# Kernel optimization log

Hardware: AMD Instinct MI355X
Metric: run time of the kernel (lower is better)

## Reference

```python
import jax, jax.numpy as jnp
import numpy as np

B, S, H, E = 4, 4096, 4096, 64
TOP_K = 2


def setup_inputs() -> dict:
    key = jax.random.key(0)
    k1, k2 = jax.random.split(key)
    x = jax.random.normal(k1, (B, S, H), dtype=jnp.float32)
    # nn.Linear weight: [num_experts, hidden_size]
    gate_w = jax.random.normal(k2, (E, H), dtype=jnp.float32) * (1.0 / np.sqrt(H))
    return {"x": x, "gate_w": gate_w}


def reference(x, gate_w):
    # gate linear: [B,S,H] @ [H,E] -> [B,S,E]
    router_logits = jnp.einsum("bsh,eh->bse", x, gate_w)
    router_weights = jax.nn.softmax(router_logits, axis=-1)
    topk_weights, topk_indices = jax.lax.top_k(router_weights, TOP_K)  # [B,S,2]
    topk_weights = topk_weights / jnp.sum(topk_weights, axis=-1, keepdims=True)
    return topk_weights, topk_indices
```

## Files before the change

### kernel.cpp

```cpp
#include <hip/hip_runtime.h>
#include <math.h>


constexpr int Hdim = 4096;
constexpr int Edim = 64;
constexpr int BM   = 64;
constexpr int BK   = 64;
constexpr int LSTR = 66;
constexpr int PSTR = 68;
constexpr int NKT  = Hdim / BK;
constexpr int NTOK = 16384;

__global__ __launch_bounds__(256)
void router_kernel(const float* __restrict__ x,
                   const float* __restrict__ gw,
                   float* __restrict__ out)
{
    __shared__ float lx[2 * BM * LSTR];
    __shared__ float lw[2 * Edim * LSTR];

    const int tid = threadIdx.x;
    const int t0  = blockIdx.x * BM;

    const int srow = tid >> 4;
    const int scol = (tid & 15) << 2;

    const int wave = tid >> 6, lane = tid & 63;
    const int tg = ((wave >> 1) << 3) + (lane >> 3);
    const int eg = ((wave & 1) << 3) + (lane & 7);

    float acc[4][4];
    #pragma unroll
    for (int i = 0; i < 4; ++i)
        #pragma unroll
        for (int j = 0; j < 4; ++j) acc[i][j] = 0.f;

    const float* xg = x + (size_t)t0 * Hdim;

    float4 rx[4], rw[4];
    #pragma unroll
    for (int m = 0; m < 4; ++m) {
        const int r = m * 16 + srow;
        rx[m] = *(const float4*)(xg + (size_t)r * Hdim + scol);
        rw[m] = *(const float4*)(gw + (size_t)r * Hdim + scol);
    }
    #pragma unroll
    for (int m = 0; m < 4; ++m) {
        const int r = m * 16 + srow;
        float2* px = (float2*)&lx[r * LSTR + scol];
        px[0] = make_float2(rx[m].x, rx[m].y);
        px[1] = make_float2(rx[m].z, rx[m].w);
        float2* pw = (float2*)&lw[r * LSTR + scol];
        pw[0] = make_float2(rw[m].x, rw[m].y);
        pw[1] = make_float2(rw[m].z, rw[m].w);
    }
    __syncthreads();

    for (int kt = 0; kt < NKT; ++kt) {
        const int cur = (kt & 1) ? BM * LSTR : 0;
        const int nxt = (kt & 1) ? 0 : BM * LSTR;
        const int knext = (kt + 1 < NKT) ? (kt + 1) * BK : 0;

        #pragma unroll
        for (int m = 0; m < 4; ++m) {
            const int r = m * 16 + srow;
            rx[m] = *(const float4*)(xg + (size_t)r * Hdim + knext + scol);
            rw[m] = *(const float4*)(gw + (size_t)r * Hdim + knext + scol);
        }

        const float* __restrict__ bx = &lx[cur];
        const float* __restrict__ bw = &lw[cur];
        #pragma unroll 8
        for (int k = 0; k < BK; k += 2) {
            float2 xa[4], wb[4];
            #pragma unroll
            for (int i = 0; i < 4; ++i)
                xa[i] = *(const float2*)&bx[(4 * tg + i) * LSTR + k];
            #pragma unroll
            for (int j = 0; j < 4; ++j)
                wb[j] = *(const float2*)&bw[(4 * eg + j) * LSTR + k];
            #pragma unroll
            for (int i = 0; i < 4; ++i)
                #pragma unroll
                for (int j = 0; j < 4; ++j)
                    acc[i][j] = fmaf(xa[i].y, wb[j].y,
                                 fmaf(xa[i].x, wb[j].x, acc[i][j]));
        }

        #pragma unroll
        for (int m = 0; m < 4; ++m) {
            const int r = m * 16 + srow;
            float2* px = (float2*)&lx[nxt + r * LSTR + scol];
            px[0] = make_float2(rx[m].x, rx[m].y);
            px[1] = make_float2(rx[m].z, rx[m].w);
            float2* pw = (float2*)&lw[nxt + r * LSTR + scol];
            pw[0] = make_float2(rw[m].x, rw[m].y);
            pw[1] = make_float2(rw[m].z, rw[m].w);
        }
        __syncthreads();
    }

    float* lg = lx;
    #pragma unroll
    for (int i = 0; i < 4; ++i) {
        float4 v = make_float4(acc[i][0], acc[i][1], acc[i][2], acc[i][3]);
        *(float4*)&lg[(4 * tg + i) * PSTR + 4 * eg] = v;
    }
    __syncthreads();

    if (tid < BM) {
        const float* row = &lg[tid * PSTR];
        float m1 = -INFINITY, m2 = -INFINITY;
        int i1 = 0, i2 = 0;
        for (int e = 0; e < Edim; ++e) {
            float v = row[e];
            if (v > m1) { m2 = m1; i2 = i1; m1 = v; i1 = e; }
            else if (v > m2) { m2 = v; i2 = e; }
        }
        const float r   = expf(m2 - m1);
        const float inv = 1.f / (1.f + r);
        const int t = t0 + tid;
        float* ow = out + 2 * (size_t)t;
        ow[0] = inv;
        ow[1] = r * inv;
        float* oi = out + 2 * (size_t)NTOK + 2 * (size_t)t;
        oi[0] = (float)i1;
        oi[1] = (float)i2;
    }
}

extern "C" void kernel_launch(void* const* d_in, const int* in_sizes, int n_in,
                              void* d_out, int out_size, void* d_ws, size_t ws_size,
                              hipStream_t stream) {
    const float* x  = (const float*)d_in[0];
    const float* gw = (const float*)d_in[1];
    float* out = (float*)d_out;
    dim3 grid(NTOK / BM), block(256);
    hipLaunchKernelGGL(router_kernel, grid, block, 0, stream, x, gw, out);
}
```

Measured before the change: 460.1 us.

## Compute router GEMM with split-fp16 MFMA instead of scalar FP32 FMAs

Replaces the scalar FP32 FMA inner loop with 16x16x32 fp16 MFMA instructions. Each FP32 input is split into a high fp16 part and a scaled low fp16 residual, and four MFMA products per tile are recombined so the result stays close to FP32 accuracy. Shared memory is reorganised into XOR-swizzled fp16 tiles to avoid bank conflicts. This trades extra conversion ALU work and four times the MFMA count for much higher matrix throughput, but it risks precision differences that could flip top-k ties.

```diff
diff --git a/kernel.cpp b/kernel.cpp
--- a/kernel.cpp
+++ b/kernel.cpp
@@ -1,115 +1,169 @@
 #include <hip/hip_runtime.h>
 #include <math.h>
 
+
+typedef _Float16 half8 __attribute__((ext_vector_type(8)));
+typedef float floatx4 __attribute__((ext_vector_type(4)));
 
 constexpr int Hdim = 4096;
 constexpr int Edim = 64;
 constexpr int BM   = 64;
 constexpr int BK   = 64;
-constexpr int LSTR = 66;
-constexpr int PSTR = 68;
 constexpr int NKT  = Hdim / BK;
 constexpr int NTOK = 16384;
+constexpr int PSTR = 68;
+constexpr float SCL  = 2048.0f;
+constexpr float ISCL = 1.0f / 2048.0f;
 
 __global__ __launch_bounds__(256)
 void router_kernel(const float* __restrict__ x,
                    const float* __restrict__ gw,
                    float* __restrict__ out)
 {
-    __shared__ float lx[2 * BM * LSTR];
-    __shared__ float lw[2 * Edim * LSTR];
+    __shared__ alignas(16) _Float16 sxh[2][BM * BK];
+    __shared__ alignas(16) _Float16 sxl[2][BM * BK];
+    __shared__ alignas(16) _Float16 swh[2][BM * BK];
+    __shared__ alignas(16) _Float16 swl[2][BM * BK];
+    __shared__ float slg[BM * PSTR];
 
     const int tid = threadIdx.x;
     const int t0  = blockIdx.x * BM;
 
-    const int srow = tid >> 4;
-    const int scol = (tid & 15) << 2;
+    const int sr = tid & 63;
+    const int q4 = tid >> 6;
+    const int sw8 = sr & 7;
+    const int a0 = sr * BK + (((2 * q4)     ^ sw8) << 3);
+    const int a1 = sr * BK + (((2 * q4 + 1) ^ sw8) << 3);
 
-    const int wave = tid >> 6, lane = tid & 63;
-    const int tg = ((wave >> 1) << 3) + (lane >> 3);
-    const int eg = ((wave & 1) << 3) + (lane & 7);
+    const int wv = tid >> 6, lane = tid & 63;
+    const int ln15 = lane & 15, quad = lane >> 4;
+    const int th = (wv >> 1) * 32;
+    const int eh = (wv & 1) * 32;
 
-    float acc[4][4];
+    const float* xrow = x  + (size_t)(t0 + sr) * Hdim + q4 * 16;
+    const float* wrow = gw + (size_t)sr        * Hdim + q4 * 16;
+
+    floatx4 accm[2][2], accc[2][2], accl[2][2];
     #pragma unroll
-    for (int i = 0; i < 4; ++i)
+    for (int a = 0; a < 2; ++a)
         #pragma unroll
-        for (int j = 0; j < 4; ++j) acc[i][j] = 0.f;
-
-    const float* xg = x + (size_t)t0 * Hdim;
+        for (int b = 0; b < 2; ++b) {
+            accm[a][b] = (floatx4)0.0f;
+            accc[a][b] = (floatx4)0.0f;
+            accl[a][b] = (floatx4)0.0f;
+        }
 
     float4 rx[4], rw[4];
+
     #pragma unroll
-    for (int m = 0; m < 4; ++m) {
-        const int r = m * 16 + srow;
-        rx[m] = *(const float4*)(xg + (size_t)r * Hdim + scol);
-        rw[m] = *(const float4*)(gw + (size_t)r * Hdim + scol);
+    for (int j = 0; j < 4; ++j) {
+        rx[j] = *(const float4*)(xrow + 4 * j);
+        rw[j] = *(const float4*)(wrow + 4 * j);
     }
-    #pragma unroll
-    for (int m = 0; m < 4; ++m) {
-        const int r = m * 16 + srow;
-        float2* px = (float2*)&lx[r * LSTR + scol];
-        px[0] = make_float2(rx[m].x, rx[m].y);
-        px[1] = make_float2(rx[m].z, rx[m].w);
-        float2* pw = (float2*)&lw[r * LSTR + scol];
-        pw[0] = make_float2(rw[m].x, rw[m].y);
-        pw[1] = make_float2(rw[m].z, rw[m].w);
+    {
+        half8 hx0, hx1, lx0, lx1, hw0, hw1, lw0, lw1;
+        #pragma unroll
+        for (int j = 0; j < 4; ++j) {
+            const float* px = (const float*)&rx[j];
+            const float* pw = (const float*)&rw[j];
+            #pragma unroll
+            for (int c = 0; c < 4; ++c) {
+                const int idx = 4 * j + c, g = idx >> 3, o = idx & 7;
+                _Float16 h = (_Float16)px[c];
+                _Float16 l = (_Float16)((px[c] - (float)h) * SCL);
+                if (g == 0) { hx0[o] = h; lx0[o] = l; } else { hx1[o] = h; lx1[o] = l; }
+                h = (_Float16)pw[c];
+                l = (_Float16)((pw[c] - (float)h) * SCL);
+                if (g == 0) { hw0[o] = h; lw0[o] = l; } else { hw1[o] = h; lw1[o] = l; }
+            }
+        }
+        *(half8*)&sxh[0][a0] = hx0;  *(half8*)&sxh[0][a1] = hx1;
+        *(half8*)&sxl[0][a0] = lx0;  *(half8*)&sxl[0][a1] = lx1;
+        *(half8*)&swh[0][a0] = hw0;  *(half8*)&swh[0][a1] = hw1;
+        *(half8*)&swl[0][a0] = lw0;  *(half8*)&swl[0][a1] = lw1;
     }
     __syncthreads();
 
     for (int kt = 0; kt < NKT; ++kt) {
-        const int cur = (kt & 1) ? BM * LSTR : 0;
-        const int nxt = (kt & 1) ? 0 : BM * LSTR;
-        const int knext = (kt + 1 < NKT) ? (kt + 1) * BK : 0;
+        const int cur = kt & 1;
+        const int nxt = cur ^ 1;
+        const int kb  = (kt + 1 < NKT) ? (kt + 1) * BK : 0;
 
         #pragma unroll
-        for (int m = 0; m < 4; ++m) {
-            const int r = m * 16 + srow;
-            rx[m] = *(const float4*)(xg + (size_t)r * Hdim + knext + scol);
-            rw[m] = *(const float4*)(gw + (size_t)r * Hdim + knext + scol);
-        }
-
-        const float* __restrict__ bx = &lx[cur];
-        const float* __restrict__ bw = &lw[cur];
-        #pragma unroll 8
-        for (int k = 0; k < BK; k += 2) {
-            float2 xa[4], wb[4];
-            #pragma unroll
-            for (int i = 0; i < 4; ++i)
-                xa[i] = *(const float2*)&bx[(4 * tg + i) * LSTR + k];
-            #pragma unroll
-            for (int j = 0; j < 4; ++j)
-                wb[j] = *(const float2*)&bw[(4 * eg + j) * LSTR + k];
-            #pragma unroll
-            for (int i = 0; i < 4; ++i)
-                #pragma unroll
-                for (int j = 0; j < 4; ++j)
-                    acc[i][j] = fmaf(xa[i].y, wb[j].y,
-                                 fmaf(xa[i].x, wb[j].x, acc[i][j]));
+        for (int j = 0; j < 4; ++j) {
+            rx[j] = *(const float4*)(xrow + kb + 4 * j);
+            rw[j] = *(const float4*)(wrow + kb + 4 * j);
         }
 
         #pragma unroll
-        for (int m = 0; m < 4; ++m) {
-            const int r = m * 16 + srow;
-            float2* px = (float2*)&lx[nxt + r * LSTR + scol];
-            px[0] = make_float2(rx[m].x, rx[m].y);
-            px[1] = make_float2(rx[m].z, rx[m].w);
-            float2* pw = (float2*)&lw[nxt + r * LSTR + scol];
-            pw[0] = make_float2(rw[m].x, rw[m].y);
-            pw[1] = make_float2(rw[m].z, rw[m].w);
+        for (int kk = 0; kk < 2; ++kk) {
+            half8 ah[2], al[2], bh[2], bl[2];
+            #pragma unroll
+            for (int mt = 0; mt < 2; ++mt) {
+                const int m = th + mt * 16 + ln15;
+                const int aA = m * BK + (((kk * 4 + quad) ^ (m & 7)) << 3);
+                ah[mt] = *(const half8*)&sxh[cur][aA];
+                al[mt] = *(const half8*)&sxl[cur][aA];
+            }
+            #pragma unroll
+            for (int nt = 0; nt < 2; ++nt) {
+                const int n = eh + nt * 16 + ln15;
+                const int aB = n * BK + (((kk * 4 + quad) ^ (n & 7)) << 3);
+                bh[nt] = *(const half8*)&swh[cur][aB];
+                bl[nt] = *(const half8*)&swl[cur][aB];
+            }
+            #pragma unroll
+            for (int mt = 0; mt < 2; ++mt)
+                #pragma unroll
+                for (int nt = 0; nt < 2; ++nt) {
+                    accm[mt][nt] = __builtin_amdgcn_mfma_f32_16x16x32_f16(ah[mt], bh[nt], accm[mt][nt], 0, 0, 0);
+                    accc[mt][nt] = __builtin_amdgcn_mfma_f32_16x16x32_f16(ah[mt], bl[nt], accc[mt][nt], 0, 0, 0);
+                    accc[mt][nt] = __builtin_amdgcn_mfma_f32_16x16x32_f16(al[mt], bh[nt], accc[mt][nt], 0, 0, 0);
+                    accl[mt][nt] = __builtin_amdgcn_mfma_f32_16x16x32_f16(al[mt], bl[nt], accl[mt][nt], 0, 0, 0);
+                }
+        }
+
+        {
+            half8 hx0, hx1, lx0, lx1, hw0, hw1, lw0, lw1;
+            #pragma unroll
+            for (int j = 0; j < 4; ++j) {
+                const float* px = (const float*)&rx[j];
+                const float* pw = (const float*)&rw[j];
+                #pragma unroll
+                for (int c = 0; c < 4; ++c) {
+                    const int idx = 4 * j + c, g = idx >> 3, o = idx & 7;
+                    _Float16 h = (_Float16)px[c];
+                    _Float16 l = (_Float16)((px[c] - (float)h) * SCL);
+                    if (g == 0) { hx0[o] = h; lx0[o] = l; } else { hx1[o] = h; lx1[o] = l; }
+                    h = (_Float16)pw[c];
+                    l = (_Float16)((pw[c] - (float)h) * SCL);
+                    if (g == 0) { hw0[o] = h; lw0[o] = l; } else { hw1[o] = h; lw1[o] = l; }
+                }
+            }
+            *(half8*)&sxh[nxt][a0] = hx0;  *(half8*)&sxh[nxt][a1] = hx1;
+            *(half8*)&sxl[nxt][a0] = lx0;  *(half8*)&sxl[nxt][a1] = lx1;
+            *(half8*)&swh[nxt][a0] = hw0;  *(half8*)&swh[nxt][a1] = hw1;
+            *(half8*)&swl[nxt][a0] = lw0;  *(half8*)&swl[nxt][a1] = lw1;
         }
         __syncthreads();
     }
 
-    float* lg = lx;
     #pragma unroll
-    for (int i = 0; i < 4; ++i) {
-        float4 v = make_float4(acc[i][0], acc[i][1], acc[i][2], acc[i][3]);
-        *(float4*)&lg[(4 * tg + i) * PSTR + 4 * eg] = v;
-    }
+    for (int mt = 0; mt < 2; ++mt)
+        #pragma unroll
+        for (int nt = 0; nt < 2; ++nt)
+            #pragma unroll
+            for (int i = 0; i < 4; ++i) {
+                const float v = accm[mt][nt][i] + accc[mt][nt][i] * ISCL
+                              + accl[mt][nt][i] * (ISCL * ISCL);
+                const int r = th + mt * 16 + quad * 4 + i;
+                const int c = eh + nt * 16 + ln15;
+                slg[r * PSTR + c] = v;
+            }
     __syncthreads();
 
     if (tid < BM) {
-        const float* row = &lg[tid * PSTR];
+        const float* row = &slg[tid * PSTR];
         float m1 = -INFINITY, m2 = -INFINITY;
         int i1 = 0, i2 = 0;
         for (int e = 0; e < Edim; ++e) {
```

Result: faster. 419.6 us (-8.8%).

## Replace FP32 FMA GEMM with split-FP16 MFMA emulation loading straight from global

Applied to the files above, without the earlier changes.

Swaps the scalar FP32 LDS-tiled GEMM for matrix-core MFMA 16x16x32 f16 instructions. Each FP32 operand is split into a high and a scaled low half-precision part, and the four cross products are accumulated to emulate FP32 accuracy. Operands are loaded directly from global memory into registers with two-chunk register prefetching, so the LDS staging and per-tile barriers go away. The block tile shrinks to 32 tokens, and launch bounds request 2 blocks per SIMD. The costs are four MFMAs per product, conversion ALU work, redundant gate-weight global loads across blocks without LDS reuse, and a small accuracy risk from the split-precision scheme.

```diff
diff --git a/kernel.cpp b/kernel.cpp
--- a/kernel.cpp
+++ b/kernel.cpp
@@ -2,114 +2,123 @@
 #include <math.h>
 
 
+typedef _Float16 half8 __attribute__((ext_vector_type(8)));
+typedef float floatx4 __attribute__((ext_vector_type(4)));
+
 constexpr int Hdim = 4096;
 constexpr int Edim = 64;
-constexpr int BM   = 64;
-constexpr int BK   = 64;
-constexpr int LSTR = 66;
-constexpr int PSTR = 68;
+constexpr int BM   = 32;
+constexpr int BK   = 32;
 constexpr int NKT  = Hdim / BK;
 constexpr int NTOK = 16384;
+constexpr int PSTR = 68;
+constexpr float SCL  = 2048.0f;
+constexpr float ISCL = 1.0f / 2048.0f;
 
-__global__ __launch_bounds__(256)
+struct Chunk { float4 a0, a1, b00, b01, b10, b11; };
+
+__device__ __forceinline__ void load_chunk(const float* __restrict__ xA,
+                                           const float* __restrict__ w0,
+                                           const float* __restrict__ w1,
+                                           int k, Chunk& c) {
+    c.a0  = *(const float4*)(xA + k);
+    c.a1  = *(const float4*)(xA + k + 4);
+    c.b00 = *(const float4*)(w0 + k);
+    c.b01 = *(const float4*)(w0 + k + 4);
+    c.b10 = *(const float4*)(w1 + k);
+    c.b11 = *(const float4*)(w1 + k + 4);
+}
+
+__device__ __forceinline__ void cvt8(const float4& u, const float4& v,
+                                     half8& h, half8& l) {
+    const float* pu = (const float*)&u;
+    const float* pv = (const float*)&v;
+    #pragma unroll
+    for (int c = 0; c < 4; ++c) {
+        _Float16 hh = (_Float16)pu[c];
+        h[c] = hh;
+        l[c] = (_Float16)((pu[c] - (float)hh) * SCL);
+        hh = (_Float16)pv[c];
+        h[4 + c] = hh;
+        l[4 + c] = (_Float16)((pv[c] - (float)hh) * SCL);
+    }
+}
+
+__device__ __forceinline__ void do_mfma(const Chunk& c, floatx4 accm[2],
+                                        floatx4 accc[2], floatx4 accl[2]) {
+    half8 ah, al, bh0, bl0, bh1, bl1;
+    cvt8(c.a0,  c.a1,  ah,  al);
+    cvt8(c.b00, c.b01, bh0, bl0);
+    cvt8(c.b10, c.b11, bh1, bl1);
+    accm[0] = __builtin_amdgcn_mfma_f32_16x16x32_f16(ah, bh0, accm[0], 0, 0, 0);
+    accc[0] = __builtin_amdgcn_mfma_f32_16x16x32_f16(ah, bl0, accc[0], 0, 0, 0);
+    accc[0] = __builtin_amdgcn_mfma_f32_16x16x32_f16(al, bh0, accc[0], 0, 0, 0);
+    accl[0] = __builtin_amdgcn_mfma_f32_16x16x32_f16(al, bl0, accl[0], 0, 0, 0);
+    accm[1] = __builtin_amdgcn_mfma_f32_16x16x32_f16(ah, bh1, accm[1], 0, 0, 0);
+    accc[1] = __builtin_amdgcn_mfma_f32_16x16x32_f16(ah, bl1, accc[1], 0, 0, 0);
+    accc[1] = __builtin_amdgcn_mfma_f32_16x16x32_f16(al, bh1, accc[1], 0, 0, 0);
+    accl[1] = __builtin_amdgcn_mfma_f32_16x16x32_f16(al, bl1, accl[1], 0, 0, 0);
+}
+
+__global__ __launch_bounds__(256, 2)
 void router_kernel(const float* __restrict__ x,
                    const float* __restrict__ gw,
                    float* __restrict__ out)
 {
-    __shared__ float lx[2 * BM * LSTR];
-    __shared__ float lw[2 * Edim * LSTR];
+    __shared__ float slg[BM * PSTR];
 
-    const int tid = threadIdx.x;
-    const int t0  = blockIdx.x * BM;
+    const int tid  = threadIdx.x;
+    const int t0   = blockIdx.x * BM;
+    const int wv   = tid >> 6, lane = tid & 63;
+    const int ln15 = lane & 15, quad = lane >> 4;
+    const int th   = (wv >> 1) * 16;
+    const int eh   = (wv & 1) * 32;
 
-    const int srow = tid >> 4;
-    const int scol = (tid & 15) << 2;
+    const float* xA = x  + (size_t)(t0 + th + ln15) * Hdim + quad * 8;
+    const float* w0 = gw + (size_t)(eh + ln15)      * Hdim + quad * 8;
+    const float* w1 = gw + (size_t)(eh + 16 + ln15) * Hdim + quad * 8;
 
-    const int wave = tid >> 6, lane = tid & 63;
-    const int tg = ((wave >> 1) << 3) + (lane >> 3);
-    const int eg = ((wave & 1) << 3) + (lane & 7);
-
-    float acc[4][4];
+    floatx4 accm[2], accc[2], accl[2];
     #pragma unroll
-    for (int i = 0; i < 4; ++i)
-        #pragma unroll
-        for (int j = 0; j < 4; ++j) acc[i][j] = 0.f;
-
-    const float* xg = x + (size_t)t0 * Hdim;
-
-    float4 rx[4], rw[4];
-    #pragma unroll
-    for (int m = 0; m < 4; ++m) {
-        const int r = m * 16 + srow;
-        rx[m] = *(const float4*)(xg + (size_t)r * Hdim + scol);
-        rw[m] = *(const float4*)(gw + (size_t)r * Hdim + scol);
-    }
-    #pragma unroll
-    for (int m = 0; m < 4; ++m) {
-        const int r = m * 16 + srow;
-        float2* px = (float2*)&lx[r * LSTR + scol];
-        px[0] = make_float2(rx[m].x, rx[m].y);
-        px[1] = make_float2(rx[m].z, rx[m].w);
-        float2* pw = (float2*)&lw[r * LSTR + scol];
-        pw[0] = make_float2(rw[m].x, rw[m].y);
-        pw[1] = make_float2(rw[m].z, rw[m].w);
-    }
-    __syncthreads();
-
-    for (int kt = 0; kt < NKT; ++kt) {
-        const int cur = (kt & 1) ? BM * LSTR : 0;
-        const int nxt = (kt & 1) ? 0 : BM * LSTR;
-        const int knext = (kt + 1 < NKT) ? (kt + 1) * BK : 0;
-
-        #pragma unroll
-        for (int m = 0; m < 4; ++m) {
-            const int r = m * 16 + srow;
-            rx[m] = *(const float4*)(xg + (size_t)r * Hdim + knext + scol);
-            rw[m] = *(const float4*)(gw + (size_t)r * Hdim + knext + scol);
-        }
-
-        const float* __restrict__ bx = &lx[cur];
-        const float* __restrict__ bw = &lw[cur];
-        #pragma unroll 8
-        for (int k = 0; k < BK; k += 2) {
-            float2 xa[4], wb[4];
-            #pragma unroll
-            for (int i = 0; i < 4; ++i)
-                xa[i] = *(const float2*)&bx[(4 * tg + i) * LSTR + k];
-            #pragma unroll
-            for (int j = 0; j < 4; ++j)
-                wb[j] = *(const float2*)&bw[(4 * eg + j) * LSTR + k];
-            #pragma unroll
-            for (int i = 0; i < 4; ++i)
-                #pragma unroll
-                for (int j = 0; j < 4; ++j)
-                    acc[i][j] = fmaf(xa[i].y, wb[j].y,
-                                 fmaf(xa[i].x, wb[j].x, acc[i][j]));
-        }
-
-        #pragma unroll
-        for (int m = 0; m < 4; ++m) {
-            const int r = m * 16 + srow;
-            float2* px = (float2*)&lx[nxt + r * LSTR + scol];
-            px[0] = make_float2(rx[m].x, rx[m].y);
-            px[1] = make_float2(rx[m].z, rx[m].w);
-            float2* pw = (float2*)&lw[nxt + r * LSTR + scol];
-            pw[0] = make_float2(rw[m].x, rw[m].y);
-            pw[1] = make_float2(rw[m].z, rw[m].w);
-        }
-        __syncthreads();
+    for (int n = 0; n < 2; ++n) {
+        accm[n] = (floatx4)0.0f;
+        accc[n] = (floatx4)0.0f;
+        accl[n] = (floatx4)0.0f;
     }
 
-    float* lg = lx;
+    Chunk c0, c1;
+    load_chunk(xA, w0, w1, 0,  c0);
+    load_chunk(xA, w0, w1, BK, c1);
+
+    for (int kt = 0; kt < NKT; kt += 2) {
+        {
+            Chunk t = c0;
+            const int kn = (kt + 2 < NKT) ? (kt + 2) * BK : kt * BK;
+            load_chunk(xA, w0, w1, kn, c0);
+            do_mfma(t, accm, accc, accl);
+        }
+        {
+            Chunk t = c1;
+            const int kn = (kt + 3 < NKT) ? (kt + 3) * BK : kt * BK;
+            load_chunk(xA, w0, w1, kn, c1);
+            do_mfma(t, accm, accc, accl);
+        }
+    }
+
     #pragma unroll
-    for (int i = 0; i < 4; ++i) {
-        float4 v = make_float4(acc[i][0], acc[i][1], acc[i][2], acc[i][3]);
-        *(float4*)&lg[(4 * tg + i) * PSTR + 4 * eg] = v;
-    }
+    for (int nt = 0; nt < 2; ++nt)
+        #pragma unroll
+        for (int i = 0; i < 4; ++i) {
+            const float v = accm[nt][i] + accc[nt][i] * ISCL
+                          + accl[nt][i] * (ISCL * ISCL);
+            const int r = th + quad * 4 + i;
+            const int cc = eh + nt * 16 + ln15;
+            slg[r * PSTR + cc] = v;
+        }
     __syncthreads();
 
     if (tid < BM) {
-        const float* row = &lg[tid * PSTR];
+        const float* row = &slg[tid * PSTR];
         float m1 = -INFINITY, m2 = -INFINITY;
         int i1 = 0, i2 = 0;
         for (int e = 0; e < Edim; ++e) {
```

New measurement: 720.8 us. +56.7%, slower.
